# Performance work log

Measured on AMD Instinct MI355X. Metric: run time of the kernel, lower is better.

The kernel has to match this reference:

```python
import jax, jax.numpy as jnp
import numpy as np

B, C_IN, FH, TW = 64, 8, 128, 128
FBINS, A, M_ARR, M_SRC = 257, 360, 4, 2
EPS = 1e-6


def _conv2d(x, w):
    return jax.lax.conv_general_dilated(x, w, (1, 1), 'SAME', dimension_numbers=('NCHW', 'OIHW', 'NCHW'))


def _bn(x, g, b, m, v):
    sh = (1, -1, 1, 1)
    return (x - m.reshape(sh)) * jax.lax.rsqrt(v.reshape(sh) + 1e-5) * g.reshape(sh) + b.reshape(sh)


def _pool2(x):
    b_, c, h, w = x.shape
    return x.reshape(b_, c, h // 2, 2, w // 2, 2).max(axis=(3, 5))


def _block(x, w, g, b, m, v):
    return _pool2(jax.nn.relu(_bn(_conv2d(x, w), g, b, m, v)))


def _conv1d(x, w, b):
    return jax.lax.conv_general_dilated(x, w, (1,), 'SAME', dimension_numbers=('NCH', 'OIH', 'NCH')) + b[None, :, None]


def setup_inputs() -> dict:
    ks = jax.random.split(jax.random.key(0), 16)
    r = lambda i, shp, s=1.0: jax.random.normal(ks[i], shp, dtype=jnp.float32) * s
    d = {
        'X': r(0, (B, C_IN, FH, TW)),
        'sv_real': r(1, (B, FBINS, A, M_ARR)),
        'sv_imag': r(2, (B, FBINS, A, M_ARR)),
        'correlation': jnp.zeros((1,), jnp.float32),
        'conv1_w': r(3, (64, C_IN, 3, 3), 0.1),
        'conv2_w': r(4, (64, 64, 3, 3), 0.04),
        'conv3_w': r(5, (64, 64, 3, 3), 0.04),
        'conv4_w': r(6, (FBINS, 64, 3, 3), 0.04),
        'fc_w': r(7, (32, 64), 0.1),
        'fc_b': jnp.zeros((32,), jnp.float32),
        'convs2_w': r(8, (FBINS, FBINS, 3), 0.02),
        'convs2_b': jnp.zeros((FBINS,), jnp.float32),
        'convs1_w': r(9, (1, FBINS, 3), 0.03),
        'convs1_b': jnp.zeros((1,), jnp.float32),
        'ca_w1': r(10, (16, FBINS), 0.06),
        'ca_w2': r(11, (FBINS, 16), 0.2),
    }
    for i, c in [(1, 64), (2, 64), (3, 64), (4, FBINS)]:
        d[f'bn{i}_g'] = jnp.ones((c,), jnp.float32)
        d[f'bn{i}_b'] = jnp.zeros((c,), jnp.float32)
        d[f'bn{i}_m'] = jnp.zeros((c,), jnp.float32)
        d[f'bn{i}_v'] = jnp.ones((c,), jnp.float32)
    return d


def reference(X, sv_real, sv_imag, correlation,
              conv1_w, bn1_g, bn1_b, bn1_m, bn1_v,
              conv2_w, bn2_g, bn2_b, bn2_m, bn2_v,
              conv3_w, bn3_g, bn3_b, bn3_m, bn3_v,
              conv4_w, bn4_g, bn4_b, bn4_m, bn4_v,
              fc_w, fc_b, convs2_w, convs2_b, convs1_w, convs1_b,
              ca_w1, ca_w2):
    b_ = X.shape[0]
    # CNN encoder: (B,8,128,128) -> (B,257,8,8)
    z = _block(X, conv1_w, bn1_g, bn1_b, bn1_m, bn1_v)
    z = _block(z, conv2_w, bn2_g, bn2_b, bn2_m, bn2_v)
    z = _block(z, conv3_w, bn3_g, bn3_b, bn3_m, bn3_v)
    z = _block(z, conv4_w, bn4_g, bn4_b, bn4_m, bn4_v)
    z = z.reshape(b_, FBINS, -1) @ fc_w.T + fc_b            # (B,257,32)
    z = z.reshape(b_, FBINS, C_IN // 2, C_IN)               # (B,257,4,8)
    Rz = jax.lax.complex(z[..., :M_ARR], z[..., M_ARR:])    # (B,257,4,4)
    # hermitianize + diagonal loading
    Rz = 0.5 * (Rz + jnp.conj(jnp.swapaxes(Rz, -1, -2)))
    Rz = Rz + 1e-5 * jnp.eye(M_ARR, dtype=Rz.dtype)
    _, evecs = jnp.linalg.eigh(Rz)                          # ascending eigenvalues
    Un = evecs[..., ::-1][..., M_SRC:]                      # noise subspace (B,F,4,2)
    UnUnH = Un @ jnp.conj(jnp.swapaxes(Un, -1, -2))         # (B,F,4,4)
    svc = jnp.conj(jax.lax.complex(sv_real, sv_imag))       # (B,F,A,4)
    # faithful to torch code: denom[a] = sum_{m,n} conj(sv[a,m]) UnUnH[m,n] conj(sv[a,n])
    denom = jnp.real(jnp.einsum('bfam,bfmn,bfan->bfa', svc, UnUnH, svc))
    spectrum = 1.0 / jnp.maximum(denom, EPS)                # (B,257,360)
    spectrum = jax.nn.leaky_relu(_conv1d(spectrum, convs2_w, convs2_b), 0.1)
    # channel attention over the 257 freq channels
    y = spectrum.mean(-1)                                   # (B,257)
    att = jax.nn.sigmoid(jax.nn.relu(y @ ca_w1.T) @ ca_w2.T)
    spectrum = spectrum * att[:, :, None]
    spectrum = jax.nn.sigmoid(_conv1d(spectrum, convs1_w, convs1_b))[:, 0, :]  # (B,360)
    # soft-argmax over top-5 peaks
    angles = jnp.linspace(0.0, 360.0, A + 1)[:-1]
    vals, idx = jax.lax.top_k(spectrum, 5)
    wts = jax.nn.softmax(20.0 * vals, axis=-1)
    doa = (wts * angles[idx]).sum(-1)[:, None]              # (B,1)
    return doa, spectrum
```

## Files before the change

kernel.cpp:

```cpp
#include <hip/hip_runtime.h>

typedef unsigned short u16;
typedef unsigned int u32;
typedef short short8 __attribute__((ext_vector_type(8)));
typedef float f32x4 __attribute__((ext_vector_type(4)));

#define NB 64
#define NFB 257
#define NANG 360

__device__ __forceinline__ u16 f2bf(float x) {
    u32 u = __float_as_uint(x);
    u = (u + 0x7fffu + ((u >> 16) & 1u)) >> 16;
    return (u16)u;
}
__device__ __forceinline__ float bf2f(u16 h) { return __uint_as_float(((u32)h) << 16); }


__global__ __launch_bounds__(256) void bnprep(
    const float* g1, const float* b1, const float* m1, const float* v1,
    const float* g2, const float* b2, const float* m2, const float* v2,
    const float* g3, const float* b3, const float* m3, const float* v3,
    const float* g4, const float* b4, const float* m4, const float* v4,
    float* out)
{
    int L = blockIdx.x;
    const float* gs[4] = {g1, g2, g3, g4};
    const float* bs[4] = {b1, b2, b3, b4};
    const float* ms[4] = {m1, m2, m3, m4};
    const float* vs[4] = {v1, v2, v3, v4};
    int n = (L == 3) ? 257 : 64;
    float* sc = out + L * 1024;
    float* bi = sc + 512;
    for (int i = threadIdx.x; i < n; i += 256) {
        float s = gs[L][i] * rsqrtf(vs[L][i] + 1e-5f);
        sc[i] = s;
        bi[i] = bs[L][i] - ms[L][i] * s;
    }
}

__global__ __launch_bounds__(256) void bpack(
    const float* __restrict__ w, u16* __restrict__ Bp,
    int CREAL, int OCREAL, int NT, int KCC, int NFTOT)
{
    int i = blockIdx.x * 256 + threadIdx.x;
    int total = NT * KCC * 2 * NFTOT * 64;
    if (i >= total) return;
    int lane = i & 63;
    int t = i >> 6;
    int nf = t % NFTOT;
    int th = t / NFTOT;
    int h = th & 1;
    int chunk = th >> 1;
    int s = chunk / KCC, kc = chunk % KCC;
    int n = nf * 16 + (lane & 15);
    int k0 = kc * 32 + (lane >> 4) * 8;
    u16 o8[8];
    #pragma unroll
    for (int e = 0; e < 8; ++e) {
        int k = k0 + e;
        float v = 0.f;
        if (k < CREAL && n < OCREAL) v = w[((size_t)n * CREAL + k) * NT + s];
        u16 hh = f2bf(v);
        o8[e] = (h == 0) ? hh : f2bf(v - bf2f(hh));
    }
    u16* d = Bp + (size_t)i * 8;
    #pragma unroll
    for (int e = 0; e < 8; ++e) d[e] = o8[e];
}

__global__ __launch_bounds__(256) void bpack1(const float* __restrict__ w, u16* __restrict__ Bp)
{
    int i = blockIdx.x * 256 + threadIdx.x;
    if (i >= 3 * 2 * 4 * 64) return;
    int lane = i & 63;
    int t = i >> 6;
    int nf = t % 4;
    int th = t / 4;
    int h = th & 1;
    int ky = th >> 1;
    int n = nf * 16 + (lane & 15);
    int q = lane >> 4;
    u16 o8[8];
    #pragma unroll
    for (int e = 0; e < 8; ++e) {
        float v = (q < 3) ? w[((size_t)(n * 8 + e) * 3 + ky) * 3 + q] : 0.f;
        u16 hh = f2bf(v);
        o8[e] = (h == 0) ? hh : f2bf(v - bf2f(hh));
    }
    u16* d = Bp + (size_t)i * 8;
    #pragma unroll
    for (int e = 0; e < 8; ++e) d[e] = o8[e];
}

__global__ __launch_bounds__(256) void xpack_kernel(
    const float* __restrict__ X, u16* __restrict__ xp)
{
    __shared__ float Xs[8][132];
    int bid = blockIdx.x;
    int prow = bid % 130;
    int b = bid / 130;
    bool inr = (prow >= 1 && prow <= 128);
    for (int i = threadIdx.x; i < 8 * 130; i += 256) {
        int c = i / 130, pcol = i % 130;
        float v = 0.f;
        if (inr && pcol >= 1 && pcol <= 128)
            v = X[(((size_t)b * 8 + c) * 128 + (prow - 1)) * 128 + (pcol - 1)];
        Xs[c][pcol] = v;
    }
    __syncthreads();
    for (int p = threadIdx.x; p < 130; p += 256) {
        short8 h8, l8;
        #pragma unroll
        for (int c = 0; c < 8; ++c) {
            float f = Xs[c][p];
            u16 hh = f2bf(f);
            h8[c] = (short)hh;
            l8[c] = (short)f2bf(f - bf2f(hh));
        }
        size_t o = (((size_t)b * 130 + prow) * 130 + p) * 16;
        *(short8*)(xp + o) = h8;
        *(short8*)(xp + o + 8) = l8;
    }
}

__global__ __launch_bounds__(256) void zpad(
    u32* buf, int Bn, int Hp, int Wp, int wpp, int doCols)
{
    int perB = 2 * Wp + (doCols ? 2 * (Hp - 2) : 0);
    long total = (long)Bn * perB * wpp;
    for (long idx = blockIdx.x * 256L + threadIdx.x; idx < total; idx += (long)gridDim.x * 256) {
        int w = (int)(idx % wpp);
        long t = idx / wpp;
        int p = (int)(t % perB);
        int b = (int)(t / perB);
        int row, col;
        if (p < Wp) { row = 0; col = p; }
        else if (p < 2 * Wp) { row = Hp - 1; col = p - Wp; }
        else { int pp = p - 2 * Wp; row = 1 + (pp >> 1); col = (pp & 1) ? (Wp - 1) : 0; }
        buf[(((size_t)b * Hp + row) * Wp + col) * (size_t)wpp + w] = 0;
    }
}

__global__ __launch_bounds__(256) void conv_c1(
    const u16* __restrict__ A, const u16* __restrict__ Bp,
    const float* __restrict__ esc, const float* __restrict__ ebi,
    u16* __restrict__ O)
{
    constexpr int Wst = 130, Hp = 130;
    constexpr int SROWS = 5;
    constexpr int SPIX = SROWS * Wst;
    __shared__ __align__(16) char sm[SPIX * 48];

    int bid = blockIdx.x;
    int ytile = bid % 64;
    int b = bid / 64;
    int y0 = ytile * 2;
    int tid = threadIdx.x;
    int wv = tid >> 6;
    int l = tid & 63;
    int r = l & 15, q = l >> 4;

    for (int i = tid; i < SPIX * 2; i += 256) {
        int pix = i >> 1, sub = i & 1;
        int prow = y0 + pix / Wst, pcol = pix % Wst;
        uint4 v = {0, 0, 0, 0};
        if (prow < Hp)
            v = *(const uint4*)(A + (((size_t)b * Hp + prow) * Wst + pcol) * 16 + sub * 8);
        *(uint4*)(sm + pix * 48 + sub * 16) = v;
    }
    __syncthreads();

    f32x4 acc[4][4] = {};

    #pragma unroll
    for (int ky = 0; ky < 3; ++ky) {
        short8 bh[4], bl[4];
        #pragma unroll
        for (int ni = 0; ni < 4; ++ni) {
            const u16* bt = Bp + ((size_t)(ky * 2) * 4 + ni) * 512 + l * 8;
            bh[ni] = *(const short8*)bt;
            bl[ni] = *(const short8*)(bt + 4 * 512);
        }
        short8 ah[4], al[4];
        #pragma unroll
        for (int mi = 0; mi < 4; ++mi) {
            int pf = wv * 2 + (mi >> 1);
            int y = mi & 1;
            int p = (y + ky) * Wst + pf * 16 + r + q;
            ah[mi] = *(const short8*)(sm + p * 48);
            al[mi] = *(const short8*)(sm + p * 48 + 16);
        }
        #pragma unroll
        for (int ni = 0; ni < 4; ++ni)
            #pragma unroll
            for (int mi = 0; mi < 4; ++mi) {
                acc[mi][ni] = __builtin_amdgcn_mfma_f32_16x16x32_bf16(ah[mi], bh[ni], acc[mi][ni], 0, 0, 0);
                acc[mi][ni] = __builtin_amdgcn_mfma_f32_16x16x32_bf16(ah[mi], bl[ni], acc[mi][ni], 0, 0, 0);
                acc[mi][ni] = __builtin_amdgcn_mfma_f32_16x16x32_bf16(al[mi], bh[ni], acc[mi][ni], 0, 0, 0);
            }
    }

    #pragma unroll
    for (int ni = 0; ni < 4; ++ni) {
        int oc = ni * 16 + r;
        float sc0 = esc[oc], bi0 = ebi[oc];
        #pragma unroll
        for (int pi = 0; pi < 2; ++pi) {
            int pf = wv * 2 + pi;
            #pragma unroll
            for (int k = 0; k < 2; ++k) {
                float m = -3.4e38f;
                #pragma unroll
                for (int dmi = 0; dmi < 2; ++dmi)
                    #pragma unroll
                    for (int dj = 0; dj < 2; ++dj)
                        m = fmaxf(m, fmaf(acc[2 * pi + dmi][ni][2 * k + dj], sc0, bi0));
                m = fmaxf(m, 0.f);
                int x2 = pf * 8 + q * 2 + k;
                size_t base = (((size_t)b * 66 + (y0 / 2 + 1)) * 66 + (x2 + 1)) * 128;
                u16* d = O + base + ((oc >> 5) << 6) + (oc & 31);
                u16 hh = f2bf(m);
                d[0] = hh;
                d[32] = f2bf(m - bf2f(hh));
            }
        }
    }
}

template<int H, int W, int OC, int R, int NF, int MFW, int OUTMODE, int NFTOT>
__global__ __launch_bounds__(256) void conv_gemm(
    const u16* __restrict__ A, const u16* __restrict__ Bp,
    const float* __restrict__ esc, const float* __restrict__ ebi,
    u16* __restrict__ O, float* __restrict__ Of)
{
    constexpr int Wst = W + 2, Hp = H + 2;
    constexpr int SROWS = R + 2;
    constexpr int SPIX = SROWS * Wst;
    constexpr int XF = W / 16;
    constexpr int HT = H / R;
    __shared__ __align__(16) char sm[SPIX * 128];

    int bid = blockIdx.x;
    int ytile = bid % HT;
    int b = bid / HT;
    int tid = threadIdx.x;
    int wv = tid >> 6;
    int l = tid & 63;
    int r = l & 15, q = l >> 4;
    int y0 = ytile * R;
    int nfg0 = blockIdx.y * NF;

    f32x4 acc[MFW][NF] = {};
    short8 Bh[2][NF], Bl[2][NF];

    auto loadB = [&](int buf, int chunk) {
        #pragma unroll
        for (int ni = 0; ni < NF; ++ni) {
            const u16* bt = Bp + ((size_t)(chunk * 2) * NFTOT + nfg0 + ni) * 512 + l * 8;
            Bh[buf][ni] = *(const short8*)bt;
            Bl[buf][ni] = *(const short8*)(bt + (size_t)NFTOT * 512);
        }
    };
    loadB(0, 0);

    #pragma unroll
    for (int cs = 0; cs < 2; ++cs) {
        __syncthreads();
        for (int i = tid; i < SPIX * 8; i += 256) {
            int pix = i >> 3, sub = i & 7;
            int prow = y0 + pix / Wst, pcol = pix % Wst;
            uint4 v = {0, 0, 0, 0};
            if (prow < Hp)
                v = *(const uint4*)(A + (((size_t)b * Hp + prow) * Wst + pcol) * 128 + cs * 64 + sub * 8);
            *(uint4*)(sm + pix * 128 + ((sub ^ (pix & 7)) << 4)) = v;
        }
        __syncthreads();

        #pragma unroll
        for (int s = 0; s < 9; ++s) {
            int cur = (cs * 9 + s) & 1;
            if (s < 8) loadB(cur ^ 1, (s + 1) * 2 + cs);
            else if (cs == 0) loadB(cur ^ 1, 1);
            int ky = s / 3, kx = s % 3;
            short8 ah[MFW], al[MFW];
            #pragma unroll
            for (int mi = 0; mi < MFW; ++mi) {
                int pf = wv * (MFW / 2) + (mi >> 1);
                int y = (pf / XF) * 2 + (mi & 1);
                int xf = pf % XF;
                int p = (y + ky) * Wst + xf * 16 + kx + r;
                int off = p * 128 + ((q ^ (p & 7)) << 4);
                ah[mi] = *(const short8*)(sm + off);
                al[mi] = *(const short8*)(sm + (off ^ 64));
            }
            #pragma unroll
            for (int ni = 0; ni < NF; ++ni)
                #pragma unroll
                for (int mi = 0; mi < MFW; ++mi) {
                    acc[mi][ni] = __builtin_amdgcn_mfma_f32_16x16x32_bf16(ah[mi], Bh[cur][ni], acc[mi][ni], 0, 0, 0);
                    acc[mi][ni] = __builtin_amdgcn_mfma_f32_16x16x32_bf16(ah[mi], Bl[cur][ni], acc[mi][ni], 0, 0, 0);
                    acc[mi][ni] = __builtin_amdgcn_mfma_f32_16x16x32_bf16(al[mi], Bh[cur][ni], acc[mi][ni], 0, 0, 0);
                }
        }
    }

    #pragma unroll
    for (int ni = 0; ni < NF; ++ni) {
        int oc = (nfg0 + ni) * 16 + r;
        float sc0 = esc[oc], bi0 = ebi[oc];
        #pragma unroll
        for (int pi = 0; pi < MFW / 2; ++pi) {
            int pf = wv * (MFW / 2) + pi;
            int y2 = y0 / 2 + pf / XF;
            int xb = (pf % XF) * 8 + q * 2;
            #pragma unroll
            for (int k = 0; k < 2; ++k) {
                float m = -3.4e38f;
                #pragma unroll
                for (int dmi = 0; dmi < 2; ++dmi)
                    #pragma unroll
                    for (int dj = 0; dj < 2; ++dj)
                        m = fmaxf(m, fmaf(acc[2 * pi + dmi][ni][2 * k + dj], sc0, bi0));
                m = fmaxf(m, 0.f);
                int x2 = xb + k;
                if (OUTMODE == 0) {
                    size_t base = (((size_t)b * (H / 2 + 2) + y2 + 1) * (W / 2 + 2) + (x2 + 1)) * 128;
                    u16* d = O + base + ((oc >> 5) << 6) + (oc & 31);
                    u16 hh = f2bf(m);
                    d[0] = hh;
                    d[32] = f2bf(m - bf2f(hh));
                } else {
                    if (oc < OC)
                        Of[(((size_t)b * (H / 2) + y2) * (W / 2) + x2) * (size_t)OC + oc] = m;
                }
            }
        }
    }
}

__global__ __launch_bounds__(256) void convs2_gemm(
    const u16* __restrict__ A, const u16* __restrict__ Bp,
    const float* __restrict__ bia, float* __restrict__ sp2)
{
    constexpr int SPIX = 194;
    __shared__ __align__(16) char sm[SPIX * 128];

    int bid = blockIdx.x;
    int tt = bid & 1;
    int b = bid >> 1;
    int nt = blockIdx.y;
    int t0 = tt * 192;
    int tid = threadIdx.x;
    int wv = tid >> 6;
    int l = tid & 63;
    int r = l & 15, q = l >> 4;

    f32x4 acc[3][3] = {};
    short8 Bh[2][3], Bl[2][3];

    auto loadB = [&](int buf, int chunk) {
        #pragma unroll
        for (int ni = 0; ni < 3; ++ni) {
            const u16* bt = Bp + ((size_t)(chunk * 2) * 18 + nt * 3 + ni) * 512 + l * 8;
            Bh[buf][ni] = *(const short8*)bt;
            Bl[buf][ni] = *(const short8*)(bt + 18 * 512);
        }
    };
    loadB(0, 0);

    #pragma unroll
    for (int cs = 0; cs < 9; ++cs) {
        __syncthreads();
        for (int i = tid; i < SPIX * 8; i += 256) {
            int pix = i >> 3, sub = i & 7;
            int gp = t0 + pix;
            uint4 v = {0, 0, 0, 0};
            if (gp < 362)
                v = *(const uint4*)(A + ((size_t)b * 362 + gp) * 576 + cs * 64 + sub * 8);
            *(uint4*)(sm + pix * 128 + ((sub ^ (pix & 7)) << 4)) = v;
        }
        __syncthreads();

        #pragma unroll
        for (int ky = 0; ky < 3; ++ky) {
            int cur = (cs * 3 + ky) & 1;
            if (ky < 2) loadB(cur ^ 1, (ky + 1) * 9 + cs);
            else if (cs < 8) loadB(cur ^ 1, cs + 1);
            #pragma unroll
            for (int mi = 0; mi < 3; ++mi) {
                int p = (wv * 3 + mi) * 16 + r + ky;
                int off = p * 128 + ((q ^ (p & 7)) << 4);
                short8 ah = *(const short8*)(sm + off);
                short8 al = *(const short8*)(sm + (off ^ 64));
                #pragma unroll
                for (int ni = 0; ni < 3; ++ni) {
                    acc[mi][ni] = __builtin_amdgcn_mfma_f32_16x16x32_bf16(ah, Bh[cur][ni], acc[mi][ni], 0, 0, 0);
                    acc[mi][ni] = __builtin_amdgcn_mfma_f32_16x16x32_bf16(ah, Bl[cur][ni], acc[mi][ni], 0, 0, 0);
                    acc[mi][ni] = __builtin_amdgcn_mfma_f32_16x16x32_bf16(al, Bh[cur][ni], acc[mi][ni], 0, 0, 0);
                }
            }
        }
    }

    #pragma unroll
    for (int ni = 0; ni < 3; ++ni) {
        int n = (nt * 3 + ni) * 16 + r;
        if (n >= NFB) continue;
        float bi0 = bia[n];
        #pragma unroll
        for (int mi = 0; mi < 3; ++mi) {
            int tb = t0 + (wv * 3 + mi) * 16 + q * 4;
            #pragma unroll
            for (int j = 0; j < 4; ++j) {
                int t = tb + j;
                if (t < NANG) {
                    float v = acc[mi][ni][j] + bi0;
                    sp2[((size_t)b * NANG + t) * NFB + n] = (v >= 0.f) ? v : 0.1f * v;
                }
            }
        }
    }
}

__global__ __launch_bounds__(256) void fc_kernel(
    const float* __restrict__ z, const float* __restrict__ fw,
    const float* __restrict__ fb, float* __restrict__ zfc)
{
    int bid = blockIdx.x;
    int ftile = bid % 33;
    int b = bid / 33;
    int j = threadIdx.x & 31;
    int f = ftile * 8 + (threadIdx.x >> 5);
    if (f >= 257) return;
    const float* zb = z + (size_t)b * 16448;
    float a = fb[j];
    #pragma unroll 8
    for (int s = 0; s < 64; ++s) a = fmaf(zb[s * 257 + f], fw[j * 64 + s], a);
    zfc[((size_t)b * 257 + f) * 32 + j] = a;
}

__global__ __launch_bounds__(64) void eigh_kernel(const float* __restrict__ z, double* __restrict__ rp)
{
    int idx = blockIdx.x * 64 + threadIdx.x;
    if (idx >= NB * NFB) return;
    const float* zr = z + (size_t)idx * 32;
    double Ar[4][4], Ai[4][4], Vr[4][4], Vi[4][4];
    #pragma unroll
    for (int m = 0; m < 4; ++m)
        #pragma unroll
        for (int n = 0; n < 4; ++n) {
            Ar[m][n] = 0.5 * ((double)zr[m * 8 + n] + (double)zr[n * 8 + m]);
            Ai[m][n] = 0.5 * ((double)zr[m * 8 + n + 4] - (double)zr[n * 8 + m + 4]);
            Vr[m][n] = (m == n) ? 1.0 : 0.0;
            Vi[m][n] = 0.0;
        }
    #pragma unroll
    for (int m = 0; m < 4; ++m) Ar[m][m] += 1e-5;

    for (int sweep = 0; sweep < 8; ++sweep) {
        #pragma unroll
        for (int p = 0; p < 3; ++p)
            #pragma unroll
            for (int qq = p + 1; qq < 4; ++qq) {
                double apr = Ar[p][qq], api = Ai[p][qq];
                double rmod = sqrt(apr * apr + api * api);
                if (rmod < 1e-300) continue;
                double cph = apr / rmod, sph = api / rmod;
                double tau = (Ar[qq][qq] - Ar[p][p]) / (2.0 * rmod);
                double t = (tau >= 0.0) ? (-1.0 / (tau + sqrt(1.0 + tau * tau)))
                                        : (1.0 / (-tau + sqrt(1.0 + tau * tau)));
                double c = 1.0 / sqrt(1.0 + t * t);
                double s = t * c;
                double wr = s * cph, wi = s * sph;
                #pragma unroll
                for (int i = 0; i < 4; ++i) {
                    double xr = Ar[i][p], xi = Ai[i][p];
                    double yr = Ar[i][qq], yi = Ai[i][qq];
                    Ar[i][p] = c * xr + (wr * yr + wi * yi);
                    Ai[i][p] = c * xi + (wr * yi - wi * yr);
                    Ar[i][qq] = c * yr - (wr * xr - wi * xi);
                    Ai[i][qq] = c * yi - (wr * xi + wi * xr);
                }
                #pragma unroll
                for (int i = 0; i < 4; ++i) {
                    double xr = Ar[p][i], xi = Ai[p][i];
                    double yr = Ar[qq][i], yi = Ai[qq][i];
                    Ar[p][i] = c * xr + (wr * yr - wi * yi);
                    Ai[p][i] = c * xi + (wr * yi + wi * yr);
                    Ar[qq][i] = c * yr - (wr * xr + wi * xi);
                    Ai[qq][i] = c * yi - (wr * xi - wi * xr);
                }
                #pragma unroll
                for (int i = 0; i < 4; ++i) {
                    double xr = Vr[i][p], xi = Vi[i][p];
                    double yr = Vr[i][qq], yi = Vi[i][qq];
                    Vr[i][p] = c * xr + (wr * yr + wi * yi);
                    Vi[i][p] = c * xi + (wr * yi - wi * yr);
                    Vr[i][qq] = c * yr - (wr * xr - wi * xi);
                    Vi[i][qq] = c * yi - (wr * xi + wi * xr);
                }
            }
    }
    double ev[4] = {Ar[0][0], Ar[1][1], Ar[2][2], Ar[3][3]};
    int i0 = 0;
    #pragma unroll
    for (int k = 1; k < 4; ++k) if (ev[k] < ev[i0]) i0 = k;
    int i1 = (i0 == 0) ? 1 : 0;
    #pragma unroll
    for (int k = 0; k < 4; ++k) if (k != i0 && ev[k] < ev[i1]) i1 = k;
    double* o = rp + (size_t)idx * 16;
    #pragma unroll
    for (int m = 0; m < 4; ++m)
        #pragma unroll
        for (int n = 0; n < 4; ++n)
            o[m * 4 + n] = Vr[m][i0] * Vr[n][i0] + Vi[m][i0] * Vi[n][i0]
                         + Vr[m][i1] * Vr[n][i1] + Vi[m][i1] * Vi[n][i1];
}

__global__ __launch_bounds__(256) void music_kernel(
    const float4* __restrict__ svr, const float4* __restrict__ svi,
    const double* __restrict__ rp, u16* __restrict__ mu)
{
    __shared__ double P[32][16];
    __shared__ float T[32][33];
    int bid = blockIdx.x;
    int at = bid % 12; bid /= 12;
    int ft = bid % 9;
    int b = bid / 9;
    int f0 = ft * 32, a0 = at * 32;
    int tid = threadIdx.x;
    for (int i = tid; i < 32 * 16; i += 256) {
        int fi = i >> 4, j = i & 15;
        int f = f0 + fi;
        P[fi][j] = (f < 257) ? rp[((size_t)b * 257 + f) * 16 + j] : 0.0;
    }
    __syncthreads();
    int asub = tid & 31, fsub = tid >> 5;
    int a = a0 + asub;
    #pragma unroll
    for (int k2 = 0; k2 < 4; ++k2) {
        int fl = fsub + 8 * k2;
        int f = f0 + fl;
        float val = 0.f;
        if (a < 360 && f < 257) {
            float4 u = svr[((size_t)b * 257 + f) * 360 + a];
            float4 w = svi[((size_t)b * 257 + f) * 360 + a];
            const double* Pf = P[fl];
            double ua[4] = {u.x, u.y, u.z, u.w};
            double wa[4] = {w.x, w.y, w.z, w.w};
            double qa = 0.0, qb = 0.0;
            #pragma unroll
            for (int m = 0; m < 4; ++m)
                #pragma unroll
                for (int n = 0; n < 4; ++n) {
                    double pmn = Pf[m * 4 + n];
                    qa += pmn * ua[m] * ua[n];
                    qb += pmn * wa[m] * wa[n];
                }
            double den = qa - qb;
            val = (float)(1.0 / fmax(den, 1e-6));
        }
        T[asub][fl] = val;
    }
    __syncthreads();
    int sec0 = f0 >> 5;
    #pragma unroll
    for (int p = 0; p < 4; ++p) {
        int row = p * 8 + (tid >> 5);
        int fc = tid & 31;
        int a2 = a0 + row;
        if (a2 < 360) {
            float v = T[row][fc];
            u16* d = mu + ((size_t)b * 362 + a2 + 1) * 576 + (size_t)sec0 * 64 + fc;
            u16 hh = f2bf(v);
            d[0] = hh;
            d[32] = f2bf(v - bf2f(hh));
        }
    }
}

__global__ __launch_bounds__(256) void attn_partial(const float* __restrict__ sp2, float* __restrict__ part)
{
    int bid = blockIdx.x;
    int ch = bid % 6;
    int b = bid / 6;
    int t0 = ch * 60;
    for (int f = threadIdx.x; f < 257; f += 256) {
        float s = 0.f;
        for (int t = 0; t < 60; ++t) s += sp2[((size_t)b * 360 + t0 + t) * 257 + f];
        part[((size_t)b * 6 + ch) * 257 + f] = s;
    }
}

__global__ __launch_bounds__(256) void attn_finish(
    const float* __restrict__ part, const float* __restrict__ w1,
    const float* __restrict__ w2, float* __restrict__ att)
{
    __shared__ float ys[257];
    __shared__ float hs[16];
    int b = blockIdx.x;
    int tid = threadIdx.x;
    for (int f = tid; f < 257; f += 256) {
        float s = 0.f;
        #pragma unroll
        for (int c = 0; c < 6; ++c) s += part[((size_t)b * 6 + c) * 257 + f];
        ys[f] = s * (1.0f / 360.0f);
    }
    __syncthreads();
    if (tid < 16) {
        float h = 0.f;
        for (int c = 0; c < 257; ++c) h = fmaf(ys[c], w1[(size_t)tid * 257 + c], h);
        hs[tid] = fmaxf(h, 0.f);
    }
    __syncthreads();
    for (int o = tid; o < 257; o += 256) {
        float a = 0.f;
        #pragma unroll
        for (int j = 0; j < 16; ++j) a = fmaf(hs[j], w2[(size_t)o * 16 + j], a);
        att[(size_t)b * 257 + o] = 1.0f / (1.0f + expf(-a));
    }
}

__global__ __launch_bounds__(256) void convs1_kernel(
    const float* __restrict__ sp2, const float* __restrict__ att,
    const float* __restrict__ w, const float* __restrict__ bb,
    float* __restrict__ outS)
{
    int bid = blockIdx.x;
    int tt = bid % 90;
    int b = bid / 90;
    int wv = threadIdx.x >> 6, l = threadIdx.x & 63;
    int t = tt * 4 + wv;
    float s = 0.f;
    for (int f = l; f < 257; f += 64) {
        float av = att[(size_t)b * 257 + f];
        float w0 = w[f * 3] * av, w1 = w[f * 3 + 1] * av, w2 = w[f * 3 + 2] * av;
        const float* col = sp2 + (size_t)b * 360 * 257 + f;
        if (t > 0)   s = fmaf(w0, col[(size_t)(t - 1) * 257], s);
        s = fmaf(w1, col[(size_t)t * 257], s);
        if (t < 359) s = fmaf(w2, col[(size_t)(t + 1) * 257], s);
    }
    #pragma unroll
    for (int off = 32; off > 0; off >>= 1) s += __shfl_down(s, off, 64);
    if (l == 0) outS[(size_t)b * 360 + t] = 1.0f / (1.0f + expf(-(s + bb[0])));
}

__global__ __launch_bounds__(64) void doa_kernel(const float* __restrict__ spec, float* __restrict__ doa)
{
    int b = blockIdx.x;
    int l = threadIdx.x;
    const float* s = spec + (size_t)b * NANG;
    float v[6];
    #pragma unroll
    for (int j = 0; j < 6; ++j) {
        int idx = l + 64 * j;
        v[j] = (idx < NANG) ? s[idx] : -3.4e38f;
    }
    float wvv[5]; int wii[5];
    #pragma unroll
    for (int k = 0; k < 5; ++k) {
        float bv = v[0]; int bj = 0;
        #pragma unroll
        for (int j = 1; j < 6; ++j)
            if (v[j] > bv) { bv = v[j]; bj = j; }
        int bi = l + 64 * bj;
        #pragma unroll
        for (int off = 1; off < 64; off <<= 1) {
            float ov = __shfl_xor(bv, off, 64);
            int oi = __shfl_xor(bi, off, 64);
            if (ov > bv || (ov == bv && oi < bi)) { bv = ov; bi = oi; }
        }
        wvv[k] = bv; wii[k] = bi;
        if ((bi & 63) == l) {
            int j = bi >> 6;
            #pragma unroll
            for (int jj = 0; jj < 6; ++jj)
                if (jj == j) v[jj] = -3.4e38f;
        }
    }
    if (l == 0) {
        float m = wvv[0];
        float wsum = 0.f, asum = 0.f;
        #pragma unroll
        for (int k = 0; k < 5; ++k) {
            float e = expf(20.0f * (wvv[k] - m));
            wsum += e;
            asum += e * (float)wii[k];
        }
        doa[b] = asum / wsum;
    }
}

extern "C" void kernel_launch(void* const* d_in, const int* in_sizes, int n_in,
                              void* d_out, int out_size, void* d_ws, size_t ws_size,
                              hipStream_t stream)
{
    const float* X    = (const float*)d_in[0];
    const float* svr  = (const float*)d_in[1];
    const float* svi  = (const float*)d_in[2];
    const float* c1w  = (const float*)d_in[4];
    const float* c2w  = (const float*)d_in[5];
    const float* c3w  = (const float*)d_in[6];
    const float* c4w  = (const float*)d_in[7];
    const float* fcw  = (const float*)d_in[8];
    const float* fcb  = (const float*)d_in[9];
    const float* s2w  = (const float*)d_in[10];
    const float* s2b  = (const float*)d_in[11];
    const float* s1w  = (const float*)d_in[12];
    const float* s1b  = (const float*)d_in[13];
    const float* caw1 = (const float*)d_in[14];
    const float* caw2 = (const float*)d_in[15];
    const float* bn1g = (const float*)d_in[16]; const float* bn1b = (const float*)d_in[17];
    const float* bn1m = (const float*)d_in[18]; const float* bn1v = (const float*)d_in[19];
    const float* bn2g = (const float*)d_in[20]; const float* bn2b = (const float*)d_in[21];
    const float* bn2m = (const float*)d_in[22]; const float* bn2v = (const float*)d_in[23];
    const float* bn3g = (const float*)d_in[24]; const float* bn3b = (const float*)d_in[25];
    const float* bn3m = (const float*)d_in[26]; const float* bn3v = (const float*)d_in[27];
    const float* bn4g = (const float*)d_in[28]; const float* bn4b = (const float*)d_in[29];
    const float* bn4m = (const float*)d_in[30]; const float* bn4v = (const float*)d_in[31];

    char* wsb = (char*)d_ws;
    u16* xp = (u16*)(wsb + 0);
    u16* c3 = (u16*)(wsb + 0);
    u16* mu = (u16*)(wsb + 0);
    const size_t Bb = 34611200;
    u16*   c2  = (u16*)(wsb + Bb);
    float*  zbuf = (float*)(wsb + Bb);
    float*  zfc  = (float*)(wsb + Bb + 4210688);
    double* rp   = (double*)(wsb + Bb + 6316032);
    float*  sp2  = (float*)(wsb + Bb + 8421376);
    float*  part = (float*)(wsb + Bb + 32106496);
    float*  att  = (float*)(wsb + Bb + 32501248);
    const size_t Cb = Bb + 71368704;
    u16* c4  = (u16*)(wsb + Cb);
    u16* bp1 = (u16*)(wsb + Cb + 5308416);
    u16* bp2 = (u16*)(wsb + Cb + 5382144);
    u16* bp3 = (u16*)(wsb + Cb + 5529600);
    u16* bp4 = (u16*)(wsb + Cb + 5677056);
    u16* bp5 = (u16*)(wsb + Cb + 6414336);
    float* bns = (float*)(wsb + Cb + 7409664);

    float* outD = (float*)d_out;
    float* outS = (float*)d_out + 64;

    bnprep<<<4, 256, 0, stream>>>(bn1g, bn1b, bn1m, bn1v, bn2g, bn2b, bn2m, bn2v,
                                  bn3g, bn3b, bn3m, bn3v, bn4g, bn4b, bn4m, bn4v, bns);
    bpack1<<<6, 256, 0, stream>>>(c1w, bp1);
    bpack<<<36, 256, 0, stream>>>(c2w, bp2, 64, 64, 9, 2, 4);
    bpack<<<36, 256, 0, stream>>>(c3w, bp3, 64, 64, 9, 2, 4);
    bpack<<<180, 256, 0, stream>>>(c4w, bp4, 64, 257, 9, 2, 20);
    bpack<<<243, 256, 0, stream>>>(s2w, bp5, 257, 257, 3, 9, 18);
    xpack_kernel<<<64 * 130, 256, 0, stream>>>(X, xp);
    zpad<<<4160, 256, 0, stream>>>((u32*)c2, 64, 66, 66, 64, 1);
    zpad<<<1088, 256, 0, stream>>>((u32*)c4, 64, 18, 18, 64, 1);

    conv_c1<<<64 * 64, 256, 0, stream>>>(xp, bp1, bns, bns + 512, c2);
    zpad<<<2112, 256, 0, stream>>>((u32*)c3, 64, 34, 34, 64, 1);
    conv_gemm<64, 64, 64, 2, 4, 2, 0, 4>
        <<<dim3(64 * 32, 1), 256, 0, stream>>>(c2, bp2, bns + 1024, bns + 1536, c3, nullptr);
    conv_gemm<32, 32, 64, 4, 4, 2, 0, 4>
        <<<dim3(64 * 8, 1), 256, 0, stream>>>(c3, bp3, bns + 2048, bns + 2560, c4, nullptr);
    zpad<<<144, 256, 0, stream>>>((u32*)mu, 64, 362, 1, 288, 0);
    conv_gemm<16, 16, 257, 8, 4, 2, 1, 20>
        <<<dim3(64 * 2, 5), 256, 0, stream>>>(c4, bp4, bns + 3072, bns + 3584, nullptr, zbuf);

    fc_kernel<<<64 * 33, 256, 0, stream>>>(zbuf, fcw, fcb, zfc);
    eigh_kernel<<<NFB, 64, 0, stream>>>(zfc, rp);
    music_kernel<<<64 * 108, 256, 0, stream>>>((const float4*)svr, (const float4*)svi, rp, mu);
    convs2_gemm<<<dim3(64 * 2, 6), 256, 0, stream>>>(mu, bp5, s2b, sp2);

    attn_partial<<<64 * 6, 256, 0, stream>>>(sp2, part);
    attn_finish<<<64, 256, 0, stream>>>(part, caw1, caw2, att);
    convs1_kernel<<<64 * 90, 256, 0, stream>>>(sp2, att, s1w, s1b, outS);
    doa_kernel<<<64, 64, 0, stream>>>(outS, outD);
}
```

Measured before the change: 442.5 us.

## Prefetch next channel chunk into registers while computing current chunk in conv GEMMs

In conv_gemm and convs2_gemm, the next channel slice of the input tile is now loaded from global memory into registers before the MFMA loop for the current slice runs. It is written to shared memory only after a barrier, so load latency overlaps with compute. Each thread also issues two 16-byte loads per loop round with compile-time trip counts, which replaces the strided loop, and the first conv kernel's staging loop is unrolled the same way. The cost is extra VGPRs for the staged registers, which may lower occupancy or cause spills next to the large accumulator arrays.

```diff
diff --git a/kernel.cpp b/kernel.cpp
--- a/kernel.cpp
+++ b/kernel.cpp
@@ -8,6 +8,8 @@
 #define NB 64
 #define NFB 257
 #define NANG 360
+
+template<int V> struct IC { static constexpr int value = V; };
 
 __device__ __forceinline__ u16 f2bf(float x) {
     u32 u = __float_as_uint(x);
@@ -161,13 +163,20 @@
     int l = tid & 63;
     int r = l & 15, q = l >> 4;
 
-    for (int i = tid; i < SPIX * 2; i += 256) {
-        int pix = i >> 1, sub = i & 1;
+    #pragma unroll
+    for (int it = 0; it < 3; ++it) {
+        int pix = tid + it * 256;
         int prow = y0 + pix / Wst, pcol = pix % Wst;
-        uint4 v = {0, 0, 0, 0};
-        if (prow < Hp)
-            v = *(const uint4*)(A + (((size_t)b * Hp + prow) * Wst + pcol) * 16 + sub * 8);
-        *(uint4*)(sm + pix * 48 + sub * 16) = v;
+        uint4 v0 = {0, 0, 0, 0}, v1 = {0, 0, 0, 0};
+        if (pix < SPIX && prow < Hp) {
+            const u16* src = A + (((size_t)b * Hp + prow) * Wst + pcol) * 16;
+            v0 = *(const uint4*)src;
+            v1 = *(const uint4*)(src + 8);
+        }
+        if (pix < SPIX) {
+            *(uint4*)(sm + pix * 48) = v0;
+            *(uint4*)(sm + pix * 48 + 16) = v1;
+        }
     }
     __syncthreads();
 
@@ -239,6 +248,8 @@
     constexpr int SPIX = SROWS * Wst;
     constexpr int XF = W / 16;
     constexpr int HT = H / R;
+    constexpr int GR = SPIX * 4;
+    constexpr int ROUNDS = (GR + 255) / 256;
     __shared__ __align__(16) char sm[SPIX * 128];
 
     int bid = blockIdx.x;
@@ -262,21 +273,28 @@
             Bl[buf][ni] = *(const short8*)(bt + (size_t)NFTOT * 512);
         }
     };
+
+    #pragma unroll
+    for (int it = 0; it < ROUNDS; ++it) {
+        int idx = tid + it * 256;
+        int pix = idx >> 2, sub = idx & 3;
+        int prow = y0 + pix / Wst, pcol = pix % Wst;
+        uint4 v0 = {0, 0, 0, 0}, v1 = {0, 0, 0, 0};
+        if (idx < GR && prow < Hp) {
+            const u16* src = A + (((size_t)b * Hp + prow) * Wst + pcol) * 128 + sub * 8;
+            v0 = *(const uint4*)src;
+            v1 = *(const uint4*)(src + 32);
+        }
+        if (idx < GR) {
+            *(uint4*)(sm + pix * 128 + ((sub ^ (pix & 7)) << 4)) = v0;
+            *(uint4*)(sm + pix * 128 + (((sub + 4) ^ (pix & 7)) << 4)) = v1;
+        }
+    }
     loadB(0, 0);
-
-    #pragma unroll
-    for (int cs = 0; cs < 2; ++cs) {
-        __syncthreads();
-        for (int i = tid; i < SPIX * 8; i += 256) {
-            int pix = i >> 3, sub = i & 7;
-            int prow = y0 + pix / Wst, pcol = pix % Wst;
-            uint4 v = {0, 0, 0, 0};
-            if (prow < Hp)
-                v = *(const uint4*)(A + (((size_t)b * Hp + prow) * Wst + pcol) * 128 + cs * 64 + sub * 8);
-            *(uint4*)(sm + pix * 128 + ((sub ^ (pix & 7)) << 4)) = v;
-        }
-        __syncthreads();
-
+    __syncthreads();
+
+    auto computePhase = [&](auto csc) {
+        constexpr int cs = decltype(csc)::value;
         #pragma unroll
         for (int s = 0; s < 9; ++s) {
             int cur = (cs * 9 + s) & 1;
@@ -303,7 +321,35 @@
                     acc[mi][ni] = __builtin_amdgcn_mfma_f32_16x16x32_bf16(al[mi], Bh[cur][ni], acc[mi][ni], 0, 0, 0);
                 }
         }
-    }
+    };
+
+    uint4 r0[ROUNDS], r1[ROUNDS];
+    #pragma unroll
+    for (int it = 0; it < ROUNDS; ++it) {
+        int idx = tid + it * 256;
+        int pix = idx >> 2, sub = idx & 3;
+        int prow = y0 + pix / Wst, pcol = pix % Wst;
+        r0[it] = (uint4){0, 0, 0, 0};
+        r1[it] = (uint4){0, 0, 0, 0};
+        if (idx < GR && prow < Hp) {
+            const u16* src = A + (((size_t)b * Hp + prow) * Wst + pcol) * 128 + 64 + sub * 8;
+            r0[it] = *(const uint4*)src;
+            r1[it] = *(const uint4*)(src + 32);
+        }
+    }
+    computePhase(IC<0>{});
+    __syncthreads();
+    #pragma unroll
+    for (int it = 0; it < ROUNDS; ++it) {
+        int idx = tid + it * 256;
+        int pix = idx >> 2, sub = idx & 3;
+        if (idx < GR) {
+            *(uint4*)(sm + pix * 128 + ((sub ^ (pix & 7)) << 4)) = r0[it];
+            *(uint4*)(sm + pix * 128 + (((sub + 4) ^ (pix & 7)) << 4)) = r1[it];
+        }
+    }
+    __syncthreads();
+    computePhase(IC<1>{});
 
     #pragma unroll
     for (int ni = 0; ni < NF; ++ni) {
@@ -344,6 +390,8 @@
     const float* __restrict__ bia, float* __restrict__ sp2)
 {
     constexpr int SPIX = 194;
+    constexpr int GR = SPIX * 4;
+    constexpr int ROUNDS = 4;
     __shared__ __align__(16) char sm[SPIX * 128];
 
     int bid = blockIdx.x;
@@ -367,21 +415,43 @@
             Bl[buf][ni] = *(const short8*)(bt + 18 * 512);
         }
     };
+    uint4 g0[ROUNDS], g1[ROUNDS];
+
+    auto stageIssue = [&](int cs) {
+        #pragma unroll
+        for (int it = 0; it < ROUNDS; ++it) {
+            int idx = tid + it * 256;
+            int pix = idx >> 2, sub = idx & 3;
+            int gp = t0 + pix;
+            g0[it] = (uint4){0, 0, 0, 0};
+            g1[it] = (uint4){0, 0, 0, 0};
+            if (idx < GR && gp < 362) {
+                const u16* src = A + ((size_t)b * 362 + gp) * 576 + cs * 64 + sub * 8;
+                g0[it] = *(const uint4*)src;
+                g1[it] = *(const uint4*)(src + 32);
+            }
+        }
+    };
+    auto stageWrite = [&]() {
+        #pragma unroll
+        for (int it = 0; it < ROUNDS; ++it) {
+            int idx = tid + it * 256;
+            int pix = idx >> 2, sub = idx & 3;
+            if (idx < GR) {
+                *(uint4*)(sm + pix * 128 + ((sub ^ (pix & 7)) << 4)) = g0[it];
+                *(uint4*)(sm + pix * 128 + (((sub + 4) ^ (pix & 7)) << 4)) = g1[it];
+            }
+        }
+    };
+
+    stageIssue(0);
+    stageWrite();
     loadB(0, 0);
+    __syncthreads();
 
     #pragma unroll
     for (int cs = 0; cs < 9; ++cs) {
-        __syncthreads();
-        for (int i = tid; i < SPIX * 8; i += 256) {
-            int pix = i >> 3, sub = i & 7;
-            int gp = t0 + pix;
-            uint4 v = {0, 0, 0, 0};
-            if (gp < 362)
-                v = *(const uint4*)(A + ((size_t)b * 362 + gp) * 576 + cs * 64 + sub * 8);
-            *(uint4*)(sm + pix * 128 + ((sub ^ (pix & 7)) << 4)) = v;
-        }
-        __syncthreads();
-
+        if (cs < 8) stageIssue(cs + 1);
         #pragma unroll
         for (int ky = 0; ky < 3; ++ky) {
             int cur = (cs * 3 + ky) & 1;
@@ -400,6 +470,11 @@
                     acc[mi][ni] = __builtin_amdgcn_mfma_f32_16x16x32_bf16(al, Bh[cur][ni], acc[mi][ni], 0, 0, 0);
                 }
             }
+        }
+        __syncthreads();
+        if (cs < 8) {
+            stageWrite();
+            __syncthreads();
         }
     }
 
```

Result: faster. 425.3 us (-3.9%).
